# Kernel tuning notes

Measured on AMD Instinct MI355X. Metric: run time of the kernel, lower is better.

## Reference

```python
import jax, jax.numpy as jnp
import numpy as np

B, T, N, F = 8, 24, 207, 16
H = 64            # hidden_dim
DH = 16           # dims_hyper[-1] / node-embedding out
DA = 4 * F        # temporal attention dim_out
DS = 64           # ss_gal gcn out dim (last_ss_gal_dim)
GDEP = 2
ALPHA, BETA, GAMMA = 0.05, 0.95, 0.95
TA = 2.0


def _lin(x, w, b=None):
    y = x @ w
    return y if b is None else y + b


def gcn_hyper(x, A, W, b):
    # x: [B,N,C], A: [N,N] static. h <- a*x + g * einsum('nvc,vw->nwc', h, A)
    h = x
    outs = [h]
    for _ in range(GDEP):
        h = ALPHA * x + GAMMA * jnp.einsum('bvc,vw->bwc', h, A)
        outs.append(h)
    return _lin(jnp.concatenate(outs, axis=-1), W, b)


def gcn_gru(x, A_dyn, A_sta, W, b):
    # x: [B,N,C], A_dyn: [B,N,N], A_sta: [N,N]
    h = x
    outs = [h]
    for _ in range(GDEP):
        h = (ALPHA * x
             + BETA * jnp.einsum('bvw,bvc->bwc', A_dyn, h)     # bmm(A^T, h)
             + GAMMA * jnp.einsum('bvc,vw->bwc', h, A_sta))
        outs.append(h)
    return _lin(jnp.concatenate(outs, axis=-1), W, b)


def gcn_ssgal(x, A, W, b):
    # x: [B*,N,C], A: [B*,N,N]
    h = x
    outs = [h]
    for _ in range(GDEP):
        h = ALPHA * x + GAMMA * jnp.einsum('bvw,bvc->bwc', A, h)
        outs.append(h)
    return _lin(jnp.concatenate(outs, axis=-1), W, b)


def setup_inputs() -> dict:
    key = jax.random.key(0)
    ks = jax.random.split(key, 32)
    i = iter(range(32))
    w = lambda *s: (0.02 * jax.random.normal(ks[next(i)], s, dtype=jnp.float32))
    inp = {
        'input_sequence': jax.random.normal(ks[next(i)], (B, T, N, F), dtype=jnp.float32),
        'static_adj': jax.random.uniform(ks[next(i)], (N, N), dtype=jnp.float32),
        # hyper graph generators: mlp in = (GDEP+1)*H -> DH
        'src_gen_w': w((GDEP + 1) * H, DH), 'src_gen_b': w(DH),
        'tgt_gen_w': w((GDEP + 1) * H, DH), 'tgt_gen_b': w(DH),
        # node embeddings: F -> DH
        'src_emb_w': w(F, DH), 'src_emb_b': w(DH),
        'tgt_emb_w': w(F, DH), 'tgt_emb_b': w(DH),
        # GRU gate GCNs: mlp in = (GDEP+1)*(F+H) -> H
        'gru_z_w': w((GDEP + 1) * (F + H), H), 'gru_z_b': w(H),
        'gru_r_w': w((GDEP + 1) * (F + H), H), 'gru_r_b': w(H),
        'gru_c_w': w((GDEP + 1) * (F + H), H), 'gru_c_b': w(H),
        # temporal attention: F -> DA, score DA -> 1
        'attn_q_w': w(F, DA),
        'attn_k_w': w(F, DA), 'attn_k_b': w(DA),
        'attn_s_w': w(DA, 1),
        # ss_gal spatial gcn: (GDEP+1)*F -> DS
        'sgcn_w': w((GDEP + 1) * F, DS), 'sgcn_b': w(DS),
        # predictors
        'short_w': w(DS, F), 'short_b': w(F),
        'long_w': w(H, F), 'long_b': w(F),
        'fus_w': w(DS + H, F), 'fus_b': w(F),
    }
    return inp


def _forward(input_sequence, static_adj,
             src_gen_w, src_gen_b, tgt_gen_w, tgt_gen_b,
             src_emb_w, src_emb_b, tgt_emb_w, tgt_emb_b,
             gru_z_w, gru_z_b, gru_r_w, gru_r_b, gru_c_w, gru_c_b,
             attn_q_w, attn_k_w, attn_k_b, attn_s_w,
             sgcn_w, sgcn_b,
             short_w, short_b, long_w, long_b, fus_w, fus_b):
    batch, steps, nodes = input_sequence.shape[0], input_sequence.shape[1], input_sequence.shape[2]
    eye = jnp.eye(nodes, dtype=input_sequence.dtype)

    def cell(x_t, h):
        # x_t: [B,N,F], h: [B,N,H]
        src_ctx = gcn_hyper(h, static_adj, src_gen_w, src_gen_b)   # [B,N,DH]
        tgt_ctx = gcn_hyper(h, static_adj, tgt_gen_w, tgt_gen_b)
        s = jnp.tanh(TA * _lin(x_t, src_emb_w, src_emb_b) * src_ctx)
        t = jnp.tanh(TA * _lin(x_t, tgt_emb_w, tgt_emb_b) * tgt_ctx)
        asym = jnp.einsum('bnc,bmc->bnm', s, t) - jnp.einsum('bnc,bmc->bnm', t, s)
        adj = jax.nn.relu(jnp.tanh(TA * asym)) + eye
        adj = adj / (adj.sum(axis=-1, keepdims=True) + 1e-8)
        gi = jnp.concatenate([x_t, h], axis=-1)
        z = jax.nn.sigmoid(gcn_gru(gi, adj, static_adj, gru_z_w, gru_z_b))
        r = jax.nn.sigmoid(gcn_gru(gi, adj, static_adj, gru_r_w, gru_r_b))
        ri = jnp.concatenate([x_t, r * h], axis=-1)
        c = jnp.tanh(gcn_gru(ri, adj, static_adj, gru_c_w, gru_c_b))
        return z * h + (1.0 - z) * c

    h = jnp.zeros((batch, nodes, H), dtype=input_sequence.dtype)
    for t_step in range(0, max(1, steps - 4), 4):
        h = cell(input_sequence[:, t_step], h)

    # ss_gal branch on the last 4 steps
    recent = input_sequence[:, -4:]            # [B,4,N,F]
    target = input_sequence[:, -1]             # [B,N,F]
    # temporal attention
    q = target @ attn_q_w                      # [B,N,DA]
    k = recent @ attn_k_w + attn_k_b           # [B,4,N,DA]
    scores = jnp.tanh(q[:, None, :, None, :] + k[:, :, None, :, :])  # [B,4,N,N,DA]
    scores = jnp.squeeze(scores @ attn_s_w, axis=-1)                  # [B,4,N,N]
    attn = jax.nn.softmax(scores, axis=-1)
    dyn_adj = static_adj[None] + attn.reshape(-1, nodes, nodes)       # [B*4,N,N]
    rh = recent.reshape(-1, nodes, recent.shape[-1])                  # [B*4,N,F]
    rh = gcn_ssgal(rh, dyn_adj, sgcn_w, sgcn_b)                       # [B*4,N,DS]
    rh = jax.nn.relu(rh.reshape(batch, -1, nodes, rh.shape[-1]))      # [B,4,N,DS]
    target = jnp.sum(rh, axis=1)                                       # [B,N,DS]

    short = _lin(target, short_w, short_b)      # [B,N,F]
    h = cell(short, h)                          # final GRU step on short-term prediction
    long = _lin(h, long_w, long_b)              # [B,N,F]
    fused = _lin(jnp.concatenate([target, h], axis=-1), fus_w, fus_b)  # [B,N,F]
    return jnp.stack([short, long, fused], axis=0)  # [3,B,N,F]


def reference(input_sequence, static_adj,
              src_gen_w, src_gen_b, tgt_gen_w, tgt_gen_b,
              src_emb_w, src_emb_b, tgt_emb_w, tgt_emb_b,
              gru_z_w, gru_z_b, gru_r_w, gru_r_b, gru_c_w, gru_c_b,
              attn_q_w, attn_k_w, attn_k_b, attn_s_w,
              sgcn_w, sgcn_b,
              short_w, short_b, long_w, long_b, fus_w, fus_b):
    return _forward(input_sequence, static_adj,
                    src_gen_w, src_gen_b, tgt_gen_w, tgt_gen_b,
                    src_emb_w, src_emb_b, tgt_emb_w, tgt_emb_b,
                    gru_z_w, gru_z_b, gru_r_w, gru_r_b, gru_c_w, gru_c_b,
                    attn_q_w, attn_k_w, attn_k_b, attn_s_w,
                    sgcn_w, sgcn_b,
                    short_w, short_b, long_w, long_b, fus_w, fus_b)
```

## Files before the change

kernel.cpp:

```cpp
#include <hip/hip_runtime.h>


constexpr int B = 8, T = 24, N = 207, F = 16, H = 64, DH = 16;
constexpr int PS = 208;
constexpr float ALPHA = 0.05f, BETA = 0.95f, GAMMA = 0.95f, TA = 2.0f;
constexpr int NF = N * F;
constexpr int BNF = B * N * F;

__device__ __forceinline__ float tanh_fast(float x) { float e = __expf(2.f * x); return 1.f - 2.f / (e + 1.f); }
__device__ __forceinline__ float sigm(float x) { return 1.f / (1.f + __expf(-x)); }
__device__ __forceinline__ float tanh_pnc(float x) {
    float x2 = x * x;
    float p = x * (27.f + x2);
    float q = 27.f + 9.f * x2;
    return p * __builtin_amdgcn_rcpf(q);
}

__global__ __launch_bounds__(256) void k_build_Ts(const float* __restrict__ adj, float* __restrict__ Ts) {
    int i = blockIdx.x * 256 + threadIdx.x;
    if (i >= N * N) return;
    int w = i / N, v = i % N;
    Ts[(size_t)w * PS + v] = adj[v * N + w];
}

__global__ __launch_bounds__(256) void k_mm_sq(const float* __restrict__ Ain, float* __restrict__ Aout) {
    const float* A = Ain;
    float* O = Aout;
    int w0 = blockIdx.x * 32, v0b = blockIdx.y * 32;
    int tid = threadIdx.x;
    __shared__ float sA[2][32][33], sB[2][32][33];
    float acc[4] = {0, 0, 0, 0};
    int i0 = tid >> 5, j = tid & 31;
    int r = tid >> 3, c4 = (tid & 7) * 4;
    float4 av, bv;
    auto loadT = [&](int u0) {
        av = make_float4(0, 0, 0, 0); bv = make_float4(0, 0, 0, 0);
        int w = w0 + r, u = u0 + r;
        if (w < N) av = *(const float4*)&A[(size_t)w * PS + u0 + c4];
        if (u < N) bv = *(const float4*)&A[(size_t)u * PS + v0b + c4];
    };
    loadT(0);
    int cur = 0;
    for (int t = 0; t < 7; t++) {
        __syncthreads();
        sA[cur][r][c4] = av.x; sA[cur][r][c4 + 1] = av.y; sA[cur][r][c4 + 2] = av.z; sA[cur][r][c4 + 3] = av.w;
        sB[cur][r][c4] = bv.x; sB[cur][r][c4 + 1] = bv.y; sB[cur][r][c4 + 2] = bv.z; sB[cur][r][c4 + 3] = bv.w;
        if (t < 6) loadT((t + 1) * 32);
        __syncthreads();
#pragma unroll 8
        for (int u_ = 0; u_ < 32; u_++) {
            float bvv = sB[cur][u_][j];
#pragma unroll
            for (int k = 0; k < 4; k++) acc[k] += sA[cur][i0 + k * 8][u_] * bvv;
        }
        cur ^= 1;
    }
#pragma unroll
    for (int k = 0; k < 4; k++) {
        int w = w0 + i0 + k * 8, v = v0b + j;
        if (w < N && v < N) O[(size_t)w * PS + v] = acc[k];
    }
}

__global__ __launch_bounds__(256) void k_cell_a(
    const float* __restrict__ h, const float* __restrict__ Ts, const float* __restrict__ A2,
    const float* __restrict__ xseq, int tsel, const float* __restrict__ xbuf,
    const float* __restrict__ Wsrc, const float* __restrict__ bsrc,
    const float* __restrict__ Wtgt, const float* __restrict__ btgt,
    const float* __restrict__ Wes, const float* __restrict__ bes,
    const float* __restrict__ Wet, const float* __restrict__ bet,
    float* __restrict__ s_out, float* __restrict__ t_out, float* __restrict__ catg) {
    int b = blockIdx.y, w0 = blockIdx.x * 16;
    int tid = threadIdx.x, ty = tid >> 4, tx = tid & 15;
    __shared__ float sTs[2][16][33], sA2[2][16][33];
    __shared__ float sH[2][32][64];
    __shared__ float cat[16][193];
    __shared__ float sW[192][16];
    __shared__ float sX[16][16], sWe[16][16];
    float au[4] = {0, 0, 0, 0}, aw[4] = {0, 0, 0, 0};
    const float* hb = h + b * N * H;
    const float* xp = (tsel >= 0) ? (xseq + ((size_t)(b * T + tsel)) * NF) : (xbuf + (size_t)b * NF);
    int pidx = tid & 127;
    int pr = pidx >> 3, pc4 = (pidx & 7) * 4;
    float4 t4;
    float4 h4[2];
    int hr[2], hc[2];
#pragma unroll
    for (int k = 0; k < 2; k++) { int l4 = tid + k * 256; hr[k] = l4 >> 4; hc[k] = (l4 & 15) * 4; }
    auto loadT = [&](int v0) {
        t4 = make_float4(0, 0, 0, 0);
        const float* src = (tid < 128) ? Ts : A2;
        int w = w0 + pr;
        if (w < N) t4 = *(const float4*)&src[(size_t)w * PS + v0 + pc4];
#pragma unroll
        for (int k = 0; k < 2; k++) {
            float4 hv = make_float4(0, 0, 0, 0);
            int v = v0 + hr[k];
            if (v < N) hv = *(const float4*)&hb[(size_t)v * H + hc[k]];
            h4[k] = hv;
        }
    };
    loadT(0);
    int cur = 0;
    for (int t = 0; t < 7; t++) {
        __syncthreads();
        {
            float (*dst)[33] = (tid < 128) ? sTs[cur] : sA2[cur];
            dst[pr][pc4] = t4.x; dst[pr][pc4 + 1] = t4.y; dst[pr][pc4 + 2] = t4.z; dst[pr][pc4 + 3] = t4.w;
        }
#pragma unroll
        for (int k = 0; k < 2; k++) *(float4*)&sH[cur][hr[k]][hc[k]] = h4[k];
        if (t < 6) loadT((t + 1) * 32);
        __syncthreads();
#pragma unroll 8
        for (int v = 0; v < 32; v++) {
            float pu = sTs[cur][ty][v], pw = sA2[cur][ty][v];
#pragma unroll
            for (int j = 0; j < 4; j++) {
                float x = sH[cur][v][tx * 4 + j];
                au[j] += pu * x; aw[j] += pw * x;
            }
        }
        cur ^= 1;
    }
    int w = w0 + ty;
    bool valid = w < N;
    __syncthreads();
    if (valid) {
#pragma unroll
        for (int j = 0; j < 4; j++) {
            int c = tx * 4 + j;
            float hv = hb[w * H + c];
            float u = au[j], w2 = aw[j];
            cat[ty][c] = hv;
            cat[ty][64 + c] = ALPHA * hv + GAMMA * u;
            cat[ty][128 + c] = ALPHA * hv + ALPHA * GAMMA * u + GAMMA * GAMMA * w2;
        }
    } else {
#pragma unroll
        for (int j = 0; j < 4; j++) {
            int c = tx * 4 + j;
            cat[ty][c] = 0; cat[ty][64 + c] = 0; cat[ty][128 + c] = 0;
        }
    }
    {
        float4 wv[3];
#pragma unroll
        for (int k = 0; k < 3; k++) {
            int l4 = tid + k * 256;
            wv[k] = *(const float4*)&Wsrc[l4 * 4];
        }
        float4 xv = make_float4(0, 0, 0, 0), ev = make_float4(0, 0, 0, 0);
        int sr = 0, sc = 0;
        if (tid < 64) {
            sr = tid >> 2; sc = (tid & 3) * 4;
            int n = w0 + sr;
            if (n < N) xv = *(const float4*)&xp[(size_t)n * F + sc];
            ev = *(const float4*)&Wes[tid * 4];
        }
#pragma unroll
        for (int k = 0; k < 3; k++) {
            int l4 = tid + k * 256;
            int r = l4 >> 2, c4 = (l4 & 3) * 4;
            *(float4*)&sW[r][c4] = wv[k];
        }
        if (tid < 64) {
            *(float4*)&sX[sr][sc] = xv;
            *(float4*)&sWe[sr][sc] = ev;
        }
    }
    __syncthreads();
    if (valid) {
#pragma unroll
        for (int j = 0; j < 5; j++) {
            int c = tx * 5 + j;
            float v = (c < 16) ? sX[ty][c] : hb[w * H + (c - 16)];
            catg[((size_t)(b * N + w)) * 240 + c] = v;
        }
    }
    {
        float ctx = bsrc[tx];
#pragma unroll 8
        for (int c = 0; c < 192; c++) ctx += cat[ty][c] * sW[c][tx];
        float xe = bes[tx];
#pragma unroll
        for (int f = 0; f < 16; f++) xe += sX[ty][f] * sWe[f][tx];
        if (valid) s_out[(b * N + w) * DH + tx] = tanh_fast(TA * xe * ctx);
    }
    __syncthreads();
    {
        float4 wv[3];
#pragma unroll
        for (int k = 0; k < 3; k++) {
            int l4 = tid + k * 256;
            wv[k] = *(const float4*)&Wtgt[l4 * 4];
        }
        float4 ev = make_float4(0, 0, 0, 0);
        if (tid < 64) ev = *(const float4*)&Wet[tid * 4];
#pragma unroll
        for (int k = 0; k < 3; k++) {
            int l4 = tid + k * 256;
            int r = l4 >> 2, c4 = (l4 & 3) * 4;
            *(float4*)&sW[r][c4] = wv[k];
        }
        if (tid < 64) *(float4*)&sWe[tid >> 2][(tid & 3) * 4] = ev;
    }
    __syncthreads();
    {
        float ctx = btgt[tx];
#pragma unroll 8
        for (int c = 0; c < 192; c++) ctx += cat[ty][c] * sW[c][tx];
        float xe = bet[tx];
#pragma unroll
        for (int f = 0; f < 16; f++) xe += sX[ty][f] * sWe[f][tx];
        if (valid) t_out[(b * N + w) * DH + tx] = tanh_fast(TA * xe * ctx);
    }
}

__global__ __launch_bounds__(256) void k_cell_bP(const float* __restrict__ s_in, const float* __restrict__ t_in,
                                                 const float* __restrict__ adj, float* __restrict__ P) {
    int b = blockIdx.y, v0 = blockIdx.x * 16;
    int tid = threadIdx.x, ty = tid >> 4, tx = tid & 15;
    __shared__ float sS[N][17], sT[N][17];
    for (int l4 = tid; l4 < 828; l4 += 256) {
        float4 sv = *(const float4*)&s_in[(size_t)b * N * 16 + l4 * 4];
        float4 tv = *(const float4*)&t_in[(size_t)b * N * 16 + l4 * 4];
        int r = l4 >> 2, c = (l4 & 3) * 4;
        sS[r][c] = sv.x; sS[r][c + 1] = sv.y; sS[r][c + 2] = sv.z; sS[r][c + 3] = sv.w;
        sT[r][c] = tv.x; sT[r][c + 1] = tv.y; sT[r][c + 2] = tv.z; sT[r][c + 3] = tv.w;
    }
    __syncthreads();
    int v = v0 + ty;
    bool valid = v < N;
    int vc = valid ? v : (N - 1);
    float sv[16], tv[16];
#pragma unroll
    for (int k = 0; k < 16; k++) { sv[k] = sS[vc][k]; tv[k] = sT[vc][k]; }
    float val[13];
    float rsum = 0.f;
#pragma unroll
    for (int idx = 0; idx < 13; idx++) {
        int w = tx + 16 * idx;
        float r = 0.f;
        if (w < N) {
            float a = 0.f;
#pragma unroll
            for (int k = 0; k < 16; k++) a += sv[k] * sT[w][k] - tv[k] * sS[w][k];
            r = tanh_fast(TA * a);
            r = r > 0.f ? r : 0.f;
            if (w == v) r += 1.f;
        }
        val[idx] = r;
        rsum += r;
    }
    float tot = rsum;
    for (int d = 8; d > 0; d >>= 1) tot += __shfl_down(tot, d, 16);
    tot = __shfl(tot, 0, 16);
    float rinv = BETA / (tot + 1e-8f);
    if (valid) {
        float* Pb = P + (size_t)b * PS * PS;
#pragma unroll
        for (int idx = 0; idx < 13; idx++) {
            int w = tx + 16 * idx;
            if (w < N) Pb[(size_t)w * PS + v] = val[idx] * rinv + GAMMA * adj[v * N + w];
        }
    }
}

__global__ __launch_bounds__(256) void k_combineT(const float* __restrict__ Ain, const float* __restrict__ rs,
                                                  const float* __restrict__ Ts, float* __restrict__ Pout,
                                                  float cA, float cT) {
    int bt = blockIdx.z;
    int w0 = blockIdx.x * 32, v0 = blockIdx.y * 32;
    int tid = threadIdx.x;
    __shared__ float tile[32][33];
    __shared__ float rsv[32];
    int r = tid >> 3, c4 = (tid & 7) * 4;
    float4 a4 = make_float4(0, 0, 0, 0);
    int v = v0 + r;
    if (v < N) a4 = *(const float4*)&Ain[(size_t)bt * PS * PS + (size_t)v * PS + w0 + c4];
    tile[r][c4] = a4.x; tile[r][c4 + 1] = a4.y; tile[r][c4 + 2] = a4.z; tile[r][c4 + 3] = a4.w;
    if (tid < 32) {
        int vv = v0 + tid;
        rsv[tid] = (vv < N) ? (cA / rs[bt * N + vv]) : 0.f;
    }
    __syncthreads();
    for (int l = tid; l < 1024; l += 256) {
        int i = l >> 5, j = l & 31;
        int w = w0 + i, vv = v0 + j;
        if (w < N && vv < N)
            Pout[(size_t)bt * PS * PS + (size_t)w * PS + vv] = tile[j][i] * rsv[j] + cT * Ts[(size_t)w * PS + vv];
    }
}

__global__ __launch_bounds__(256) void k_prop1(const float* __restrict__ P, float* __restrict__ cat) {
    int b = blockIdx.y, w0 = blockIdx.x * 16, c0 = blockIdx.z * 16;
    int tid = threadIdx.x, ty = tid >> 4, tx = tid & 15;
    const float* Pb = P + (size_t)b * PS * PS;
    __shared__ float sP[2][16][33], sX[2][32][17];
    float a1 = 0.f;
    int pr = tid >> 4, pc = (tid & 15) * 2;
    int xr = tid >> 3, xc = (tid & 7) * 2;
    float2 pv, xv;
    auto loadT = [&](int v0) {
        pv = make_float2(0, 0); xv = make_float2(0, 0);
        int w = w0 + pr;
        if (w < N) pv = *(const float2*)&Pb[(size_t)w * PS + v0 + pc];
        int vv = v0 + xr;
        if (vv < N) xv = *(const float2*)&cat[((size_t)(b * N + vv)) * 240 + c0 + xc];
    };
    loadT(0);
    int cur = 0;
    for (int t = 0; t < 7; t++) {
        __syncthreads();
        sP[cur][pr][pc] = pv.x; sP[cur][pr][pc + 1] = pv.y;
        sX[cur][xr][xc] = xv.x; sX[cur][xr][xc + 1] = xv.y;
        if (t < 6) loadT((t + 1) * 32);
        __syncthreads();
#pragma unroll 8
        for (int v_ = 0; v_ < 32; v_++) a1 += sP[cur][ty][v_] * sX[cur][v_][tx];
        cur ^= 1;
    }
    int w = w0 + ty, c = c0 + tx;
    if (w < N) {
        size_t base = ((size_t)(b * N + w)) * 240;
        cat[base + 80 + c] = ALPHA * cat[base + c] + a1;
    }
}

__global__ __launch_bounds__(256) void k_gate(
    const float* __restrict__ cat, const float* __restrict__ P,
    const float* __restrict__ Wa, const float* __restrict__ ba,
    const float* __restrict__ Wb, const float* __restrict__ bb,
    int baseMode,
    const float* __restrict__ xseq, int tsel, const float* __restrict__ xbuf,
    float* __restrict__ zbuf, float* __restrict__ ricat,
    float* __restrict__ h,
    const float* __restrict__ target,
    const float* __restrict__ Wlong, const float* __restrict__ blong,
    const float* __restrict__ Wfus, const float* __restrict__ bfus,
    float* __restrict__ out) {
    int mode = baseMode + blockIdx.z;
    const float* W = (mode == 1) ? Wb : Wa;
    const float* bias = (mode == 1) ? bb : ba;
    int b = blockIdx.y, w0 = blockIdx.x * 16;
    int tid = threadIdx.x, ty = tid >> 4, tx = tid & 15;
    const float* Pb = P + (size_t)b * PS * PS;
    __shared__ float sC[16][241];
    __shared__ float sP[16][33];
    __shared__ float sX[32][81];
    __shared__ float sW[48][65];
    __shared__ float hrow[16][65], trow[16][65];
    for (int l4 = tid; l4 < 640; l4 += 256) {
        int r = l4 / 40, c4 = (l4 % 40) * 4;
        int w = w0 + r;
        float4 v4 = make_float4(0, 0, 0, 0);
        if (w < N) v4 = *(const float4*)&cat[((size_t)(b * N + w)) * 240 + c4];
        sC[r][c4] = v4.x; sC[r][c4 + 1] = v4.y; sC[r][c4 + 2] = v4.z; sC[r][c4 + 3] = v4.w;
    }
    float acc[5] = {0, 0, 0, 0, 0};
    int prr = tid >> 4, prc = (tid & 15) * 2;
    int xrow = tid & 31, xc0 = (tid >> 5) * 10;
    float2 pv;
    float2 xv[5];
    auto loadT = [&](int v0) {
        pv = make_float2(0, 0);
        int w = w0 + prr;
        if (w < N) pv = *(const float2*)&Pb[(size_t)w * PS + v0 + prc];
        int v = v0 + xrow;
#pragma unroll
        for (int k = 0; k < 5; k++) xv[k] = make_float2(0, 0);
        if (v < N) {
            const float* src = &cat[((size_t)(b * N + v)) * 240 + 80 + xc0];
#pragma unroll
            for (int k = 0; k < 5; k++) xv[k] = *(const float2*)&src[k * 2];
        }
    };
    loadT(0);
    for (int t = 0; t < 7; t++) {
        __syncthreads();
        sP[prr][prc] = pv.x; sP[prr][prc + 1] = pv.y;
#pragma unroll
        for (int k = 0; k < 5; k++) { sX[xrow][xc0 + 2 * k] = xv[k].x; sX[xrow][xc0 + 2 * k + 1] = xv[k].y; }
        if (t < 6) loadT((t + 1) * 32);
        __syncthreads();
#pragma unroll 8
        for (int v = 0; v < 32; v++) {
            float p = sP[ty][v];
#pragma unroll
            for (int j = 0; j < 5; j++) acc[j] += p * sX[v][tx * 5 + j];
        }
    }
#pragma unroll
    for (int j = 0; j < 5; j++) {
        int c = tx * 5 + j;
        sC[ty][160 + c] = ALPHA * sC[ty][c] + acc[j];
    }
    float4 wv[3];
#pragma unroll
    for (int k = 0; k < 3; k++) wv[k] = *(const float4*)&W[(tid + k * 256) * 4];
    float ga[4];
#pragma unroll
    for (int j = 0; j < 4; j++) ga[j] = bias[tx * 4 + j];
    for (int ch = 0; ch < 5; ch++) {
        __syncthreads();
#pragma unroll
        for (int k = 0; k < 3; k++) {
            int l4 = tid + k * 256;
            int r = l4 >> 4, cc = (l4 & 15) * 4;
            sW[r][cc] = wv[k].x; sW[r][cc + 1] = wv[k].y; sW[r][cc + 2] = wv[k].z; sW[r][cc + 3] = wv[k].w;
        }
        if (ch < 4) {
#pragma unroll
            for (int k = 0; k < 3; k++) wv[k] = *(const float4*)&W[(size_t)(ch + 1) * 48 * 64 + (tid + k * 256) * 4];
        }
        __syncthreads();
        int c0 = ch * 48;
#pragma unroll 8
        for (int cc = 0; cc < 48; cc++) {
            float cv = sC[ty][c0 + cc];
#pragma unroll
            for (int j = 0; j < 4; j++) ga[j] += cv * sW[cc][tx * 4 + j];
        }
    }
    int w = w0 + ty;
    bool valid = w < N;
    if (mode == 0) {
        if (valid) {
#pragma unroll
            for (int j = 0; j < 4; j++) zbuf[((size_t)(b * N + w)) * 64 + tx * 4 + j] = sigm(ga[j]);
        }
    } else if (mode == 1) {
        if (valid) {
#pragma unroll
            for (int j = 0; j < 4; j++) {
                int o = tx * 4 + j;
                ricat[((size_t)(b * N + w)) * 240 + 16 + o] = sigm(ga[j]) * h[((size_t)(b * N + w)) * 64 + o];
            }
            if (tx < 4) {
                const float* xp = (tsel >= 0) ? (xseq + ((size_t)(b * T + tsel)) * NF) : (xbuf + (size_t)b * NF);
#pragma unroll
                for (int j = 0; j < 4; j++) {
                    int c = tx * 4 + j;
                    ricat[((size_t)(b * N + w)) * 240 + c] = xp[w * F + c];
                }
            }
        }
    } else {
#pragma unroll
        for (int j = 0; j < 4; j++) {
            int o = tx * 4 + j;
            float cval = tanh_fast(ga[j]);
            float zv = 0.f, hv = 0.f;
            if (valid) { zv = zbuf[((size_t)(b * N + w)) * 64 + o]; hv = h[((size_t)(b * N + w)) * 64 + o]; }
            float hn = zv * hv + (1.f - zv) * cval;
            if (valid) h[((size_t)(b * N + w)) * 64 + o] = hn;
            hrow[ty][o] = valid ? hn : 0.f;
        }
        if (mode == 3) {
            for (int l = tid; l < 1024; l += 256) {
                int i = l >> 6, o = l & 63;
                int ww = w0 + i;
                trow[i][o] = (ww < N) ? target[((size_t)(b * N + ww)) * 64 + o] : 0.f;
            }
            __syncthreads();
            float lg = blong[tx];
            float fs = bfus[tx];
            for (int o = 0; o < 64; o++) {
                lg += hrow[ty][o] * Wlong[o * 16 + tx];
                fs += trow[ty][o] * Wfus[o * 16 + tx] + hrow[ty][o] * Wfus[(64 + o) * 16 + tx];
            }
            if (valid) {
                out[((size_t)1 * B * N + b * N + w) * 16 + tx] = lg;
                out[((size_t)2 * B * N + b * N + w) * 16 + tx] = fs;
            }
        }
    }
}

__global__ __launch_bounds__(256) void k_attn2(const float* __restrict__ inp,
                                               const float* __restrict__ Wq, const float* __restrict__ Wk,
                                               const float* __restrict__ kb, const float* __restrict__ sw_,
                                               float* __restrict__ attnU, float* __restrict__ rsum) {
    int bt = blockIdx.z, b = bt >> 2, tau = bt & 3;
    int n0 = blockIdx.x * 32, m0 = blockIdx.y * 32;
    int tid = threadIdx.x, ti = tid >> 4, tj = tid & 15;
    __shared__ float sQ[32][65], sK[32][65];
    __shared__ float sWq[16][64], sWk[16][64];
    __shared__ float sXq[32][17], sXk[32][17];
    __shared__ float ssw[64], skb[64];
    const float* xq = inp + ((size_t)(b * T + (T - 1))) * NF;
    const float* xk = inp + ((size_t)(b * T + 20 + tau)) * NF;
    {
        float4 wq4 = *(const float4*)&Wq[tid * 4];
        float4 wk4 = *(const float4*)&Wk[tid * 4];
        *(float4*)&sWq[tid >> 4][(tid & 15) * 4] = wq4;
        *(float4*)&sWk[tid >> 4][(tid & 15) * 4] = wk4;
        if (tid < 64) { ssw[tid] = sw_[tid]; skb[tid] = kb[tid]; }
        int idx = tid & 127;
        int r = idx >> 2, c4 = (idx & 3) * 4;
        if (tid < 128) {
            float4 a = make_float4(0, 0, 0, 0);
            int n = n0 + r;
            if (n < N) a = *(const float4*)&xq[(size_t)n * F + c4];
            sXq[r][c4] = a.x; sXq[r][c4 + 1] = a.y; sXq[r][c4 + 2] = a.z; sXq[r][c4 + 3] = a.w;
        } else {
            float4 c = make_float4(0, 0, 0, 0);
            int m = m0 + r;
            if (m < N) c = *(const float4*)&xk[(size_t)m * F + c4];
            sXk[r][c4] = c.x; sXk[r][c4 + 1] = c.y; sXk[r][c4 + 2] = c.z; sXk[r][c4 + 3] = c.w;
        }
    }
    __syncthreads();
    {
        int r = tid >> 3, o0 = (tid & 7) * 8;
        float xr[16], xkr[16];
#pragma unroll
        for (int f = 0; f < 16; f++) { xr[f] = sXq[r][f]; xkr[f] = sXk[r][f]; }
#pragma unroll
        for (int j = 0; j < 8; j++) {
            int o = o0 + j;
            float aq = 0.f, ak = skb[o];
#pragma unroll
            for (int f = 0; f < 16; f++) { aq += xr[f] * sWq[f][o]; ak += xkr[f] * sWk[f][o]; }
            sQ[r][o] = aq; sK[r][o] = ak;
        }
    }
    __syncthreads();
    float s00 = 0.f, s01 = 0.f, s10 = 0.f, s11 = 0.f;
#pragma unroll 2
    for (int d = 0; d < 64; d++) {
        float w = ssw[d];
        float q1 = sQ[ti][d], q2 = sQ[ti + 16][d];
        float k1 = sK[tj][d], k2 = sK[tj + 16][d];
        s00 += tanh_pnc(q1 + k1) * w;
        s01 += tanh_pnc(q1 + k2) * w;
        s10 += tanh_pnc(q2 + k1) * w;
        s11 += tanh_pnc(q2 + k2) * w;
    }
    int n1 = n0 + ti, n2 = n0 + ti + 16, m1 = m0 + tj, m2 = m0 + tj + 16;
    bool vn1 = n1 < N, vn2 = n2 < N, vm1 = m1 < N, vm2 = m2 < N;
    float e00 = (vn1 && vm1) ? __expf(s00) : 0.f;
    float e01 = (vn1 && vm2) ? __expf(s01) : 0.f;
    float e10 = (vn2 && vm1) ? __expf(s10) : 0.f;
    float e11 = (vn2 && vm2) ? __expf(s11) : 0.f;
    float part1 = e00 + e01, part2 = e10 + e11;
    for (int d = 8; d > 0; d >>= 1) {
        part1 += __shfl_down(part1, d, 16);
        part2 += __shfl_down(part2, d, 16);
    }
    if (tj == 0) {
        if (vn1) atomicAdd(&rsum[bt * N + n1], part1);
        if (vn2) atomicAdd(&rsum[bt * N + n2], part2);
    }
    size_t base = (size_t)bt * PS * PS;
    if (vn1 && vm1) attnU[base + (size_t)n1 * PS + m1] = e00;
    if (vn1 && vm2) attnU[base + (size_t)n1 * PS + m2] = e01;
    if (vn2 && vm1) attnU[base + (size_t)n2 * PS + m1] = e10;
    if (vn2 && vm2) attnU[base + (size_t)n2 * PS + m2] = e11;
}

__global__ __launch_bounds__(256) void k_prop_xr(const float* __restrict__ Pd, const float* __restrict__ inp,
                                                 float* __restrict__ x1) {
    int bt = blockIdx.y, w0 = blockIdx.x * 16;
    int b = bt >> 2, tau = bt & 3;
    const float* xb = inp + ((size_t)(b * T + 20 + tau)) * NF;
    const float* Pb = Pd + (size_t)bt * PS * PS;
    int tid = threadIdx.x, ty = tid >> 4, tx = tid & 15;
    __shared__ float sP[2][16][33];
    __shared__ float sX[2][32][17];
    float acc = 0.f;
    int prr = tid >> 3, pcc = (tid & 7) * 4;
    int xrr = (tid - 128) >> 2, xcc = ((tid - 128) & 3) * 4;
    float4 pv, xv;
    auto loadT = [&](int v0) {
        pv = make_float4(0, 0, 0, 0); xv = make_float4(0, 0, 0, 0);
        if (tid < 128) {
            int w = w0 + prr;
            if (w < N) pv = *(const float4*)&Pb[(size_t)w * PS + v0 + pcc];
        } else {
            int v = v0 + xrr;
            if (v < N) xv = *(const float4*)&xb[(size_t)v * F + xcc];
        }
    };
    loadT(0);
    int cur = 0;
    for (int t = 0; t < 7; t++) {
        __syncthreads();
        if (tid < 128) {
            sP[cur][prr][pcc] = pv.x; sP[cur][prr][pcc + 1] = pv.y; sP[cur][prr][pcc + 2] = pv.z; sP[cur][prr][pcc + 3] = pv.w;
        } else {
            sX[cur][xrr][xcc] = xv.x; sX[cur][xrr][xcc + 1] = xv.y; sX[cur][xrr][xcc + 2] = xv.z; sX[cur][xrr][xcc + 3] = xv.w;
        }
        if (t < 6) loadT((t + 1) * 32);
        __syncthreads();
#pragma unroll 8
        for (int v = 0; v < 32; v++) acc += sP[cur][ty][v] * sX[cur][v][tx];
        cur ^= 1;
    }
    int w = w0 + ty;
    if (w < N) x1[((size_t)(bt * N + w)) * 16 + tx] = ALPHA * xb[w * F + tx] + acc;
}

__global__ __launch_bounds__(256) void k_sgc2(const float* __restrict__ Pd, const float* __restrict__ x1,
                                              const float* __restrict__ inp,
                                              const float* __restrict__ Ws, const float* __restrict__ bs,
                                              float* __restrict__ target) {
    int bt = blockIdx.y, b = bt >> 2, tau = bt & 3, w0 = blockIdx.x * 16;
    const float* xb = inp + ((size_t)(b * T + 20 + tau)) * NF;
    const float* Pb = Pd + (size_t)bt * PS * PS;
    int tid = threadIdx.x, ty = tid >> 4, tx = tid & 15;
    __shared__ float sP[2][16][33], sX[2][32][17], cat[16][48], sW[48][64];
    float acc = 0.f;
    int prr = tid >> 3, pcc = (tid & 7) * 4;
    int xrr = (tid - 128) >> 2, xcc = ((tid - 128) & 3) * 4;
    float4 pv, xv;
    auto loadT = [&](int v0) {
        pv = make_float4(0, 0, 0, 0); xv = make_float4(0, 0, 0, 0);
        if (tid < 128) {
            int w = w0 + prr;
            if (w < N) pv = *(const float4*)&Pb[(size_t)w * PS + v0 + pcc];
        } else {
            int v = v0 + xrr;
            if (v < N) xv = *(const float4*)&x1[((size_t)(bt * N + v)) * 16 + xcc];
        }
    };
    loadT(0);
    int cur = 0;
    for (int t = 0; t < 7; t++) {
        __syncthreads();
        if (tid < 128) {
            sP[cur][prr][pcc] = pv.x; sP[cur][prr][pcc + 1] = pv.y; sP[cur][prr][pcc + 2] = pv.z; sP[cur][prr][pcc + 3] = pv.w;
        } else {
            sX[cur][xrr][xcc] = xv.x; sX[cur][xrr][xcc + 1] = xv.y; sX[cur][xrr][xcc + 2] = xv.z; sX[cur][xrr][xcc + 3] = xv.w;
        }
        if (t < 6) loadT((t + 1) * 32);
        __syncthreads();
#pragma unroll 8
        for (int v = 0; v < 32; v++) acc += sP[cur][ty][v] * sX[cur][v][tx];
        cur ^= 1;
    }
    int w = w0 + ty;
    bool valid = w < N;
    __syncthreads();
    for (int l = tid; l < 512; l += 256) {
        int i = l >> 5, c = l & 31;
        int ww = w0 + i;
        float vv = 0;
        if (ww < N) {
            if (c < 16) vv = xb[ww * F + c];
            else vv = x1[((size_t)bt * N + ww) * 16 + (c - 16)];
        }
        cat[i][c] = vv;
    }
    {
        float x0 = valid ? xb[w * F + tx] : 0.f;
        cat[ty][32 + tx] = ALPHA * x0 + acc;
    }
    {
        float4 wv[3];
#pragma unroll
        for (int k = 0; k < 3; k++) wv[k] = *(const float4*)&Ws[(tid + k * 256) * 4];
#pragma unroll
        for (int k = 0; k < 3; k++) {
            int l4 = tid + k * 256;
            *(float4*)&sW[l4 >> 4][(l4 & 15) * 4] = wv[k];
        }
    }
    __syncthreads();
    float a[4];
#pragma unroll
    for (int j = 0; j < 4; j++) a[j] = bs[tx * 4 + j];
#pragma unroll 8
    for (int cc = 0; cc < 48; cc++) {
        float cv = cat[ty][cc];
#pragma unroll
        for (int j = 0; j < 4; j++) a[j] += cv * sW[cc][tx * 4 + j];
    }
    if (valid) {
#pragma unroll
        for (int j = 0; j < 4; j++) {
            float r = a[j] > 0.f ? a[j] : 0.f;
            atomicAdd(&target[(b * N + w) * 64 + tx * 4 + j], r);
        }
    }
}

__global__ __launch_bounds__(256) void k_short(const float* __restrict__ target,
                                               const float* __restrict__ Wsh, const float* __restrict__ bsh,
                                               float* __restrict__ out, float* __restrict__ xshort) {
    int b = blockIdx.y, n0 = blockIdx.x * 16;
    int tid = threadIdx.x, ty = tid >> 4, tx = tid & 15;
    __shared__ float trow[16][65], sW[64][16];
    {
        int r = tid >> 4, c4 = (tid & 15) * 4;
        int n = n0 + r;
        float4 tv = make_float4(0, 0, 0, 0);
        if (n < N) tv = *(const float4*)&target[((size_t)(b * N + n)) * 64 + c4];
        trow[r][c4] = tv.x; trow[r][c4 + 1] = tv.y; trow[r][c4 + 2] = tv.z; trow[r][c4 + 3] = tv.w;
        float4 wv = *(const float4*)&Wsh[tid * 4];
        *(float4*)&sW[tid >> 2][(tid & 3) * 4] = wv;
    }
    __syncthreads();
    float a = bsh[tx];
#pragma unroll 8
    for (int o = 0; o < 64; o++) a += trow[ty][o] * sW[o][tx];
    int n = n0 + ty;
    if (n < N) {
        out[((size_t)0 * B * N + b * N + n) * 16 + tx] = a;
        xshort[(b * N + n) * 16 + tx] = a;
    }
}

extern "C" void kernel_launch(void* const* d_in, const int* in_sizes, int n_in,
                              void* d_out, int out_size, void* d_ws, size_t ws_size,
                              hipStream_t stream) {
    const float* inp = (const float*)d_in[0];
    const float* adj = (const float*)d_in[1];
    const float* src_gen_w = (const float*)d_in[2];
    const float* src_gen_b = (const float*)d_in[3];
    const float* tgt_gen_w = (const float*)d_in[4];
    const float* tgt_gen_b = (const float*)d_in[5];
    const float* src_emb_w = (const float*)d_in[6];
    const float* src_emb_b = (const float*)d_in[7];
    const float* tgt_emb_w = (const float*)d_in[8];
    const float* tgt_emb_b = (const float*)d_in[9];
    const float* gru_z_w = (const float*)d_in[10];
    const float* gru_z_b = (const float*)d_in[11];
    const float* gru_r_w = (const float*)d_in[12];
    const float* gru_r_b = (const float*)d_in[13];
    const float* gru_c_w = (const float*)d_in[14];
    const float* gru_c_b = (const float*)d_in[15];
    const float* attn_q_w = (const float*)d_in[16];
    const float* attn_k_w = (const float*)d_in[17];
    const float* attn_k_b = (const float*)d_in[18];
    const float* attn_s_w = (const float*)d_in[19];
    const float* sgcn_w = (const float*)d_in[20];
    const float* sgcn_b = (const float*)d_in[21];
    const float* short_w = (const float*)d_in[22];
    const float* short_b = (const float*)d_in[23];
    const float* long_w = (const float*)d_in[24];
    const float* long_b = (const float*)d_in[25];
    const float* fus_w = (const float*)d_in[26];
    const float* fus_b = (const float*)d_in[27];
    float* out = (float*)d_out;

    float* ws = (float*)d_ws;
    size_t off = 0;
    auto A = [&](size_t n) { n = (n + 3) & ~(size_t)3; float* p = ws + off; off += n; return p; };
    float* Ts = A((size_t)PS * PS);
    float* A2 = A((size_t)PS * PS);
    float* h = A((size_t)B * N * H);
    float* sbuf = A((size_t)B * N * DH);
    float* tbuf = A((size_t)B * N * DH);
    float* P = A((size_t)B * PS * PS);
    float* catg = A((size_t)B * N * 240);
    float* catc = A((size_t)B * N * 240);
    float* zb = A((size_t)B * N * 64);
    float* attnU = A((size_t)32 * PS * PS);
    float* Pd = A((size_t)32 * PS * PS);
    float* x1 = A((size_t)32 * NF);
    float* target = A((size_t)B * N * 64);
    float* rsum = A((size_t)32 * N);
    float* xshort = A(BNF);
    (void)ws_size; (void)in_sizes; (void)n_in; (void)out_size;

    hipMemsetAsync(h, 0, sizeof(float) * B * N * H, stream);
    hipMemsetAsync(target, 0, sizeof(float) * (B * N * 64), stream);
    hipMemsetAsync(rsum, 0, sizeof(float) * (32 * N), stream);
    k_build_Ts<<<(N * N + 255) / 256, 256, 0, stream>>>(adj, Ts);
    k_mm_sq<<<dim3(7, 7), 256, 0, stream>>>(Ts, A2);

    auto run_cell = [&](int tsel, const float* xbuf, int finalFlag) {
        k_cell_a<<<dim3(13, B), 256, 0, stream>>>(h, Ts, A2, inp, tsel, xbuf,
                                                  src_gen_w, src_gen_b, tgt_gen_w, tgt_gen_b,
                                                  src_emb_w, src_emb_b, tgt_emb_w, tgt_emb_b, sbuf, tbuf, catg);
        k_cell_bP<<<dim3(13, B), 256, 0, stream>>>(sbuf, tbuf, adj, P);
        k_prop1<<<dim3(13, B, 5), 256, 0, stream>>>(P, catg);
        k_gate<<<dim3(13, B, 2), 256, 0, stream>>>(catg, P, gru_z_w, gru_z_b, gru_r_w, gru_r_b, 0,
                                                   inp, tsel, xbuf, zb, catc, h,
                                                   nullptr, nullptr, nullptr, nullptr, nullptr, nullptr);
        k_prop1<<<dim3(13, B, 5), 256, 0, stream>>>(P, catc);
        k_gate<<<dim3(13, B, 1), 256, 0, stream>>>(catc, P, gru_c_w, gru_c_b, nullptr, nullptr, 2 + finalFlag,
                                                   nullptr, 0, nullptr, zb, nullptr, h,
                                                   target, long_w, long_b, fus_w, fus_b, out);
    };

    for (int t = 0; t < 20; t += 4) run_cell(t, nullptr, 0);

    k_attn2<<<dim3(7, 7, 32), 256, 0, stream>>>(inp, attn_q_w, attn_k_w, attn_k_b, attn_s_w, attnU, rsum);
    k_combineT<<<dim3(7, 7, 32), 256, 0, stream>>>(attnU, rsum, Ts, Pd, GAMMA, GAMMA);
    k_prop_xr<<<dim3(13, 32), 256, 0, stream>>>(Pd, inp, x1);
    k_sgc2<<<dim3(13, 32), 256, 0, stream>>>(Pd, x1, inp, sgcn_w, sgcn_b, target);
    k_short<<<dim3(13, B), 256, 0, stream>>>(target, short_w, short_b, out, xshort);

    run_cell(-1, xshort, 1);
}
```

Before: 661.6 us.

## Fuse attention combine into propagation kernels and split cell_a src/tgt across grid

Removes the k_combineT kernel: attention now writes its transposed tile directly, and the propagation kernels combine the normalized attention and static adjacency on the fly. They do this by scaling x with the reciprocal row sums and accumulating two products. k_cell_a gets a z-dimension of 2 so the source and target hyper-graph projections run in separate blocks instead of sequentially. The three memsets become one. The intent is to cut a full-size intermediate write and read and a kernel launch, and to double parallelism in the cell kernel. The cost is redundant propagation work per lane in cell_a and doubled shared and global loads in the prop kernels.

```diff
diff --git a/kernel.cpp b/kernel.cpp
--- a/kernel.cpp
+++ b/kernel.cpp
@@ -70,7 +70,7 @@
     const float* __restrict__ Wes, const float* __restrict__ bes,
     const float* __restrict__ Wet, const float* __restrict__ bet,
     float* __restrict__ s_out, float* __restrict__ t_out, float* __restrict__ catg) {
-    int b = blockIdx.y, w0 = blockIdx.x * 16;
+    int b = blockIdx.y, w0 = blockIdx.x * 16, lane = blockIdx.z;
     int tid = threadIdx.x, ty = tid >> 4, tx = tid & 15;
     __shared__ float sTs[2][16][33], sA2[2][16][33];
     __shared__ float sH[2][32][64];
@@ -130,7 +130,7 @@
 #pragma unroll
         for (int j = 0; j < 4; j++) {
             int c = tx * 4 + j;
-            float hv = hb[w * H + c];
+            float hv = hb[(size_t)w * H + c];
             float u = au[j], w2 = aw[j];
             cat[ty][c] = hv;
             cat[ty][64 + c] = ALPHA * hv + GAMMA * u;
@@ -143,20 +143,21 @@
             cat[ty][c] = 0; cat[ty][64 + c] = 0; cat[ty][128 + c] = 0;
         }
     }
+    const float* Wg = lane ? Wtgt : Wsrc;
+    const float* bg = lane ? btgt : bsrc;
+    const float* We = lane ? Wet : Wes;
+    const float* be = lane ? bet : bes;
     {
         float4 wv[3];
 #pragma unroll
-        for (int k = 0; k < 3; k++) {
-            int l4 = tid + k * 256;
-            wv[k] = *(const float4*)&Wsrc[l4 * 4];
-        }
+        for (int k = 0; k < 3; k++) wv[k] = *(const float4*)&Wg[(tid + k * 256) * 4];
         float4 xv = make_float4(0, 0, 0, 0), ev = make_float4(0, 0, 0, 0);
         int sr = 0, sc = 0;
         if (tid < 64) {
             sr = tid >> 2; sc = (tid & 3) * 4;
             int n = w0 + sr;
             if (n < N) xv = *(const float4*)&xp[(size_t)n * F + sc];
-            ev = *(const float4*)&Wes[tid * 4];
+            ev = *(const float4*)&We[tid * 4];
         }
 #pragma unroll
         for (int k = 0; k < 3; k++) {
@@ -170,50 +171,26 @@
         }
     }
     __syncthreads();
-    if (valid) {
+    if (lane == 0 && valid) {
 #pragma unroll
         for (int j = 0; j < 5; j++) {
             int c = tx * 5 + j;
-            float v = (c < 16) ? sX[ty][c] : hb[w * H + (c - 16)];
+            float v = (c < 16) ? sX[ty][c] : hb[(size_t)w * H + (c - 16)];
             catg[((size_t)(b * N + w)) * 240 + c] = v;
         }
     }
     {
-        float ctx = bsrc[tx];
+        float ctx = bg[tx];
 #pragma unroll 8
         for (int c = 0; c < 192; c++) ctx += cat[ty][c] * sW[c][tx];
-        float xe = bes[tx];
+        float xe = be[tx];
 #pragma unroll
         for (int f = 0; f < 16; f++) xe += sX[ty][f] * sWe[f][tx];
-        if (valid) s_out[(b * N + w) * DH + tx] = tanh_fast(TA * xe * ctx);
-    }
-    __syncthreads();
-    {
-        float4 wv[3];
-#pragma unroll
-        for (int k = 0; k < 3; k++) {
-            int l4 = tid + k * 256;
-            wv[k] = *(const float4*)&Wtgt[l4 * 4];
-        }
-        float4 ev = make_float4(0, 0, 0, 0);
-        if (tid < 64) ev = *(const float4*)&Wet[tid * 4];
-#pragma unroll
-        for (int k = 0; k < 3; k++) {
-            int l4 = tid + k * 256;
-            int r = l4 >> 2, c4 = (l4 & 3) * 4;
-            *(float4*)&sW[r][c4] = wv[k];
-        }
-        if (tid < 64) *(float4*)&sWe[tid >> 2][(tid & 3) * 4] = ev;
-    }
-    __syncthreads();
-    {
-        float ctx = btgt[tx];
-#pragma unroll 8
-        for (int c = 0; c < 192; c++) ctx += cat[ty][c] * sW[c][tx];
-        float xe = bet[tx];
-#pragma unroll
-        for (int f = 0; f < 16; f++) xe += sX[ty][f] * sWe[f][tx];
-        if (valid) t_out[(b * N + w) * DH + tx] = tanh_fast(TA * xe * ctx);
+        if (valid) {
+            float val = tanh_fast(TA * xe * ctx);
+            if (lane == 0) s_out[(size_t)(b * N + w) * DH + tx] = val;
+            else           t_out[(size_t)(b * N + w) * DH + tx] = val;
+        }
     }
 }
 
@@ -264,32 +241,6 @@
             int w = tx + 16 * idx;
             if (w < N) Pb[(size_t)w * PS + v] = val[idx] * rinv + GAMMA * adj[v * N + w];
         }
-    }
-}
-
-__global__ __launch_bounds__(256) void k_combineT(const float* __restrict__ Ain, const float* __restrict__ rs,
-                                                  const float* __restrict__ Ts, float* __restrict__ Pout,
-                                                  float cA, float cT) {
-    int bt = blockIdx.z;
-    int w0 = blockIdx.x * 32, v0 = blockIdx.y * 32;
-    int tid = threadIdx.x;
-    __shared__ float tile[32][33];
-    __shared__ float rsv[32];
-    int r = tid >> 3, c4 = (tid & 7) * 4;
-    float4 a4 = make_float4(0, 0, 0, 0);
-    int v = v0 + r;
-    if (v < N) a4 = *(const float4*)&Ain[(size_t)bt * PS * PS + (size_t)v * PS + w0 + c4];
-    tile[r][c4] = a4.x; tile[r][c4 + 1] = a4.y; tile[r][c4 + 2] = a4.z; tile[r][c4 + 3] = a4.w;
-    if (tid < 32) {
-        int vv = v0 + tid;
-        rsv[tid] = (vv < N) ? (cA / rs[bt * N + vv]) : 0.f;
-    }
-    __syncthreads();
-    for (int l = tid; l < 1024; l += 256) {
-        int i = l >> 5, j = l & 31;
-        int w = w0 + i, vv = v0 + j;
-        if (w < N && vv < N)
-            Pout[(size_t)bt * PS * PS + (size_t)w * PS + vv] = tile[j][i] * rsv[j] + cT * Ts[(size_t)w * PS + vv];
     }
 }
 
@@ -412,7 +363,7 @@
         }
         if (ch < 4) {
 #pragma unroll
-            for (int k = 0; k < 3; k++) wv[k] = *(const float4*)&W[(size_t)(ch + 1) * 48 * 64 + (tid + k * 256) * 4];
+            for (int k = 0; k < 3; k++) wv[k] = *(const float4*)&W[(size_t)(ch + 1) * 3072 + (tid + k * 256) * 4];
         }
         __syncthreads();
         int c0 = ch * 48;
@@ -481,7 +432,7 @@
 __global__ __launch_bounds__(256) void k_attn2(const float* __restrict__ inp,
                                                const float* __restrict__ Wq, const float* __restrict__ Wk,
                                                const float* __restrict__ kb, const float* __restrict__ sw_,
-                                               float* __restrict__ attnU, float* __restrict__ rsum) {
+                                               float* __restrict__ attnT, float* __restrict__ rsum) {
     int bt = blockIdx.z, b = bt >> 2, tau = bt & 3;
     int n0 = blockIdx.x * 32, m0 = blockIdx.y * 32;
     int tid = threadIdx.x, ti = tid >> 4, tj = tid & 15;
@@ -553,34 +504,53 @@
         if (vn1) atomicAdd(&rsum[bt * N + n1], part1);
         if (vn2) atomicAdd(&rsum[bt * N + n2], part2);
     }
-    size_t base = (size_t)bt * PS * PS;
-    if (vn1 && vm1) attnU[base + (size_t)n1 * PS + m1] = e00;
-    if (vn1 && vm2) attnU[base + (size_t)n1 * PS + m2] = e01;
-    if (vn2 && vm1) attnU[base + (size_t)n2 * PS + m1] = e10;
-    if (vn2 && vm2) attnU[base + (size_t)n2 * PS + m2] = e11;
-}
-
-__global__ __launch_bounds__(256) void k_prop_xr(const float* __restrict__ Pd, const float* __restrict__ inp,
+    __syncthreads();
+    float* tile = &sQ[0][0];
+    tile[tj * 33 + ti] = e00;
+    tile[(tj + 16) * 33 + ti] = e01;
+    tile[tj * 33 + ti + 16] = e10;
+    tile[(tj + 16) * 33 + ti + 16] = e11;
+    __syncthreads();
+    {
+        int row = tid >> 3, c4 = (tid & 7) * 4;
+        int m = m0 + row;
+        if (m < N) {
+            float4 v = make_float4(tile[row * 33 + c4], tile[row * 33 + c4 + 1],
+                                   tile[row * 33 + c4 + 2], tile[row * 33 + c4 + 3]);
+            *(float4*)&attnT[(size_t)bt * PS * PS + (size_t)m * PS + n0 + c4] = v;
+        }
+    }
+}
+
+__global__ __launch_bounds__(256) void k_prop_xr(const float* __restrict__ attnT, const float* __restrict__ rsum,
+                                                 const float* __restrict__ Ts, const float* __restrict__ inp,
                                                  float* __restrict__ x1) {
     int bt = blockIdx.y, w0 = blockIdx.x * 16;
     int b = bt >> 2, tau = bt & 3;
     const float* xb = inp + ((size_t)(b * T + 20 + tau)) * NF;
-    const float* Pb = Pd + (size_t)bt * PS * PS;
+    const float* PA = attnT + (size_t)bt * PS * PS;
     int tid = threadIdx.x, ty = tid >> 4, tx = tid & 15;
-    __shared__ float sP[2][16][33];
-    __shared__ float sX[2][32][17];
-    float acc = 0.f;
+    __shared__ float sPA[2][16][33], sPT[2][16][33];
+    __shared__ float sX[2][32][17], sXs[2][32][17];
+    float accA = 0.f, accT = 0.f;
     int prr = tid >> 3, pcc = (tid & 7) * 4;
     int xrr = (tid - 128) >> 2, xcc = ((tid - 128) & 3) * 4;
-    float4 pv, xv;
+    float4 pa, pt, xv;
+    float rinv_;
     auto loadT = [&](int v0) {
-        pv = make_float4(0, 0, 0, 0); xv = make_float4(0, 0, 0, 0);
+        pa = make_float4(0, 0, 0, 0); pt = make_float4(0, 0, 0, 0); xv = make_float4(0, 0, 0, 0); rinv_ = 0.f;
         if (tid < 128) {
             int w = w0 + prr;
-            if (w < N) pv = *(const float4*)&Pb[(size_t)w * PS + v0 + pcc];
+            if (w < N) {
+                pa = *(const float4*)&PA[(size_t)w * PS + v0 + pcc];
+                pt = *(const float4*)&Ts[(size_t)w * PS + v0 + pcc];
+            }
         } else {
             int v = v0 + xrr;
-            if (v < N) xv = *(const float4*)&xb[(size_t)v * F + xcc];
+            if (v < N) {
+                xv = *(const float4*)&xb[(size_t)v * F + xcc];
+                rinv_ = __builtin_amdgcn_rcpf(rsum[bt * N + v]);
+            }
         }
     };
     loadT(0);
@@ -588,41 +558,57 @@
     for (int t = 0; t < 7; t++) {
         __syncthreads();
         if (tid < 128) {
-            sP[cur][prr][pcc] = pv.x; sP[cur][prr][pcc + 1] = pv.y; sP[cur][prr][pcc + 2] = pv.z; sP[cur][prr][pcc + 3] = pv.w;
+            sPA[cur][prr][pcc] = pa.x; sPA[cur][prr][pcc + 1] = pa.y; sPA[cur][prr][pcc + 2] = pa.z; sPA[cur][prr][pcc + 3] = pa.w;
+            sPT[cur][prr][pcc] = pt.x; sPT[cur][prr][pcc + 1] = pt.y; sPT[cur][prr][pcc + 2] = pt.z; sPT[cur][prr][pcc + 3] = pt.w;
         } else {
             sX[cur][xrr][xcc] = xv.x; sX[cur][xrr][xcc + 1] = xv.y; sX[cur][xrr][xcc + 2] = xv.z; sX[cur][xrr][xcc + 3] = xv.w;
+            sXs[cur][xrr][xcc] = xv.x * rinv_; sXs[cur][xrr][xcc + 1] = xv.y * rinv_;
+            sXs[cur][xrr][xcc + 2] = xv.z * rinv_; sXs[cur][xrr][xcc + 3] = xv.w * rinv_;
         }
         if (t < 6) loadT((t + 1) * 32);
         __syncthreads();
 #pragma unroll 8
-        for (int v = 0; v < 32; v++) acc += sP[cur][ty][v] * sX[cur][v][tx];
+        for (int v = 0; v < 32; v++) {
+            accA += sPA[cur][ty][v] * sXs[cur][v][tx];
+            accT += sPT[cur][ty][v] * sX[cur][v][tx];
+        }
         cur ^= 1;
     }
     int w = w0 + ty;
-    if (w < N) x1[((size_t)(bt * N + w)) * 16 + tx] = ALPHA * xb[w * F + tx] + acc;
-}
-
-__global__ __launch_bounds__(256) void k_sgc2(const float* __restrict__ Pd, const float* __restrict__ x1,
+    if (w < N) x1[((size_t)(bt * N + w)) * 16 + tx] = ALPHA * xb[w * F + tx] + GAMMA * (accA + accT);
+}
+
+__global__ __launch_bounds__(256) void k_sgc2(const float* __restrict__ attnT, const float* __restrict__ rsum,
+                                              const float* __restrict__ Ts, const float* __restrict__ x1,
                                               const float* __restrict__ inp,
                                               const float* __restrict__ Ws, const float* __restrict__ bs,
                                               float* __restrict__ target) {
     int bt = blockIdx.y, b = bt >> 2, tau = bt & 3, w0 = blockIdx.x * 16;
     const float* xb = inp + ((size_t)(b * T + 20 + tau)) * NF;
-    const float* Pb = Pd + (size_t)bt * PS * PS;
+    const float* PA = attnT + (size_t)bt * PS * PS;
     int tid = threadIdx.x, ty = tid >> 4, tx = tid & 15;
-    __shared__ float sP[2][16][33], sX[2][32][17], cat[16][48], sW[48][64];
-    float acc = 0.f;
+    __shared__ float sPA[2][16][33], sPT[2][16][33];
+    __shared__ float sX[2][32][17], sXs[2][32][17];
+    __shared__ float cat[16][48], sW[48][64];
+    float accA = 0.f, accT = 0.f;
     int prr = tid >> 3, pcc = (tid & 7) * 4;
     int xrr = (tid - 128) >> 2, xcc = ((tid - 128) & 3) * 4;
-    float4 pv, xv;
+    float4 pa, pt, xv;
+    float rinv_;
     auto loadT = [&](int v0) {
-        pv = make_float4(0, 0, 0, 0); xv = make_float4(0, 0, 0, 0);
+        pa = make_float4(0, 0, 0, 0); pt = make_float4(0, 0, 0, 0); xv = make_float4(0, 0, 0, 0); rinv_ = 0.f;
         if (tid < 128) {
             int w = w0 + prr;
-            if (w < N) pv = *(const float4*)&Pb[(size_t)w * PS + v0 + pcc];
+            if (w < N) {
+                pa = *(const float4*)&PA[(size_t)w * PS + v0 + pcc];
+                pt = *(const float4*)&Ts[(size_t)w * PS + v0 + pcc];
+            }
         } else {
             int v = v0 + xrr;
-            if (v < N) xv = *(const float4*)&x1[((size_t)(bt * N + v)) * 16 + xcc];
+            if (v < N) {
+                xv = *(const float4*)&x1[((size_t)(bt * N + v)) * 16 + xcc];
+                rinv_ = __builtin_amdgcn_rcpf(rsum[bt * N + v]);
+            }
         }
     };
     loadT(0);
@@ -630,14 +616,20 @@
     for (int t = 0; t < 7; t++) {
         __syncthreads();
         if (tid < 128) {
-            sP[cur][prr][pcc] = pv.x; sP[cur][prr][pcc + 1] = pv.y; sP[cur][prr][pcc + 2] = pv.z; sP[cur][prr][pcc + 3] = pv.w;
+            sPA[cur][prr][pcc] = pa.x; sPA[cur][prr][pcc + 1] = pa.y; sPA[cur][prr][pcc + 2] = pa.z; sPA[cur][prr][pcc + 3] = pa.w;
+            sPT[cur][prr][pcc] = pt.x; sPT[cur][prr][pcc + 1] = pt.y; sPT[cur][prr][pcc + 2] = pt.z; sPT[cur][prr][pcc + 3] = pt.w;
         } else {
             sX[cur][xrr][xcc] = xv.x; sX[cur][xrr][xcc + 1] = xv.y; sX[cur][xrr][xcc + 2] = xv.z; sX[cur][xrr][xcc + 3] = xv.w;
+            sXs[cur][xrr][xcc] = xv.x * rinv_; sXs[cur][xrr][xcc + 1] = xv.y * rinv_;
+            sXs[cur][xrr][xcc + 2] = xv.z * rinv_; sXs[cur][xrr][xcc + 3] = xv.w * rinv_;
         }
         if (t < 6) loadT((t + 1) * 32);
         __syncthreads();
 #pragma unroll 8
-        for (int v = 0; v < 32; v++) acc += sP[cur][ty][v] * sX[cur][v][tx];
+        for (int v = 0; v < 32; v++) {
+            accA += sPA[cur][ty][v] * sXs[cur][v][tx];
+            accT += sPT[cur][ty][v] * sX[cur][v][tx];
+        }
         cur ^= 1;
     }
     int w = w0 + ty;
@@ -655,7 +647,7 @@
     }
     {
         float x0 = valid ? xb[w * F + tx] : 0.f;
-        cat[ty][32 + tx] = ALPHA * x0 + acc;
+        cat[ty][32 + tx] = ALPHA * x0 + GAMMA * (accA + accT);
     }
     {
         float4 wv[3];
@@ -750,31 +742,30 @@
     auto A = [&](size_t n) { n = (n + 3) & ~(size_t)3; float* p = ws + off; off += n; return p; };
     float* Ts = A((size_t)PS * PS);
     float* A2 = A((size_t)PS * PS);
-    float* h = A((size_t)B * N * H);
     float* sbuf = A((size_t)B * N * DH);
     float* tbuf = A((size_t)B * N * DH);
     float* P = A((size_t)B * PS * PS);
     float* catg = A((size_t)B * N * 240);
     float* catc = A((size_t)B * N * 240);
     float* zb = A((size_t)B * N * 64);
-    float* attnU = A((size_t)32 * PS * PS);
-    float* Pd = A((size_t)32 * PS * PS);
+    float* attnT = A((size_t)32 * PS * PS);
     float* x1 = A((size_t)32 * NF);
+    float* xshort = A(BNF);
+    size_t zero_begin = off;
+    float* h = A((size_t)B * N * H);
     float* target = A((size_t)B * N * 64);
     float* rsum = A((size_t)32 * N);
-    float* xshort = A(BNF);
+    size_t zero_end = off;
     (void)ws_size; (void)in_sizes; (void)n_in; (void)out_size;
 
-    hipMemsetAsync(h, 0, sizeof(float) * B * N * H, stream);
-    hipMemsetAsync(target, 0, sizeof(float) * (B * N * 64), stream);
-    hipMemsetAsync(rsum, 0, sizeof(float) * (32 * N), stream);
+    hipMemsetAsync(h, 0, (zero_end - zero_begin) * sizeof(float), stream);
     k_build_Ts<<<(N * N + 255) / 256, 256, 0, stream>>>(adj, Ts);
     k_mm_sq<<<dim3(7, 7), 256, 0, stream>>>(Ts, A2);
 
     auto run_cell = [&](int tsel, const float* xbuf, int finalFlag) {
-        k_cell_a<<<dim3(13, B), 256, 0, stream>>>(h, Ts, A2, inp, tsel, xbuf,
-                                                  src_gen_w, src_gen_b, tgt_gen_w, tgt_gen_b,
-                                                  src_emb_w, src_emb_b, tgt_emb_w, tgt_emb_b, sbuf, tbuf, catg);
+        k_cell_a<<<dim3(13, B, 2), 256, 0, stream>>>(h, Ts, A2, inp, tsel, xbuf,
+                                                     src_gen_w, src_gen_b, tgt_gen_w, tgt_gen_b,
+                                                     src_emb_w, src_emb_b, tgt_emb_w, tgt_emb_b, sbuf, tbuf, catg);
         k_cell_bP<<<dim3(13, B), 256, 0, stream>>>(sbuf, tbuf, adj, P);
         k_prop1<<<dim3(13, B, 5), 256, 0, stream>>>(P, catg);
         k_gate<<<dim3(13, B, 2), 256, 0, stream>>>(catg, P, gru_z_w, gru_z_b, gru_r_w, gru_r_b, 0,
@@ -788,10 +779,9 @@
 
     for (int t = 0; t < 20; t += 4) run_cell(t, nullptr, 0);
 
-    k_attn2<<<dim3(7, 7, 32), 256, 0, stream>>>(inp, attn_q_w, attn_k_w, attn_k_b, attn_s_w, attnU, rsum);
-    k_combineT<<<dim3(7, 7, 32), 256, 0, stream>>>(attnU, rsum, Ts, Pd, GAMMA, GAMMA);
-    k_prop_xr<<<dim3(13, 32), 256, 0, stream>>>(Pd, inp, x1);
-    k_sgc2<<<dim3(13, 32), 256, 0, stream>>>(Pd, x1, inp, sgcn_w, sgcn_b, target);
+    k_attn2<<<dim3(7, 7, 32), 256, 0, stream>>>(inp, attn_q_w, attn_k_w, attn_k_b, attn_s_w, attnT, rsum);
+    k_prop_xr<<<dim3(13, 32), 256, 0, stream>>>(attnT, rsum, Ts, inp, x1);
+    k_sgc2<<<dim3(13, 32), 256, 0, stream>>>(attnT, rsum, Ts, x1, inp, sgcn_w, sgcn_b, target);
     k_short<<<dim3(13, B), 256, 0, stream>>>(target, short_w, short_b, out, xshort);
 
     run_cell(-1, xshort, 1);
```

After: 645.6 us. -2.4%, faster.
